# Performance work log

Hardware: AMD Instinct MI355X
Metric: run time of the kernel (lower is better)

Reference implementation:

```python
import jax, jax.numpy as jnp
import numpy as np
import math

EMB_ATOM = 256
PAIR_IN = 64
PAIR_OUT = 64
EMB_RBF = 16
N_ATOMS = 50000
N_EDGES = 1_600_000
KMAX = 32


def setup_inputs() -> dict:
    key = jax.random.key(0)
    ks = jax.random.split(key, 8)
    h = jax.random.normal(ks[0], (N_ATOMS, EMB_ATOM), dtype=jnp.float32)
    rad_basis = jax.random.normal(ks[1], (N_ATOMS, EMB_RBF, KMAX), dtype=jnp.float32)
    edge_index = jax.random.randint(ks[2], (2, N_EDGES), 0, N_ATOMS, dtype=jnp.int64)
    target_neighbor_idx = jax.random.randint(ks[3], (N_EDGES,), 0, KMAX, dtype=jnp.int64)
    # Learned parameters (Dense layers are bias-free); stored as [in, out].
    W_down = jax.random.normal(ks[4], (EMB_ATOM, PAIR_IN), dtype=jnp.float32) / math.sqrt(EMB_ATOM)
    W_bilinear = jax.random.normal(ks[5], (EMB_RBF * PAIR_IN, PAIR_OUT), dtype=jnp.float32) / math.sqrt(EMB_RBF * PAIR_IN)
    W_up = jax.random.normal(ks[6], (PAIR_OUT, EMB_ATOM), dtype=jnp.float32) / math.sqrt(PAIR_OUT)
    scale = jnp.ones((), dtype=jnp.float32)  # ScaleFactor learned scalar
    return {"h": h, "rad_basis": rad_basis, "edge_index": edge_index,
            "target_neighbor_idx": target_neighbor_idx, "W_down": W_down,
            "W_bilinear": W_bilinear, "W_up": W_up, "scale": scale}


def reference(h, rad_basis, edge_index, target_neighbor_idx, W_down, W_bilinear, W_up, scale):
    num_atoms = h.shape[0]
    kmax = rad_basis.shape[-1]
    pair_in = W_down.shape[-1]
    # down_projection (Dense, silu activation, no bias)
    x_b = jax.nn.silu(h @ W_down)                              # [N, pair_in]
    x_ba = x_b[edge_index[0]]                                  # [E, pair_in] gather by source atom
    # scatter edge features into padded per-atom neighbor buffer
    x2 = jnp.zeros((num_atoms, kmax, pair_in), dtype=x_ba.dtype)
    x2 = x2.at[edge_index[1], target_neighbor_idx].set(x_ba)   # [N, Kmax, pair_in]
    # rbf-weighted neighbor aggregation: batched matmul
    x_ba2 = jnp.einsum('nrk,nkd->nrd', rad_basis, x2)          # [N, rbf, pair_in]
    h_out = x_ba2.reshape(num_atoms, -1) @ W_bilinear          # bilinear Dense, no activation
    h_out = h_out * scale                                      # ScaleFactor
    return jax.nn.silu(h_out @ W_up)                           # up_projection
```

## Files before the change

kernel.cpp:

```cpp
#include <hip/hip_runtime.h>

typedef __attribute__((ext_vector_type(8))) short short8;
typedef __attribute__((ext_vector_type(4))) float floatx4;
typedef unsigned short u16;
typedef unsigned int u32;
typedef unsigned long long u64;

#define KMAXN 32

__device__ __forceinline__ u16 f2b(float f) {
    unsigned u = __builtin_bit_cast(unsigned, f);
    u += 0x7FFFu + ((u >> 16) & 1u);
    return (u16)(u >> 16);
}
__device__ __forceinline__ float silu_f(float x) {
    return x / (1.f + __expf(-x));
}

__global__ __launch_bounds__(256) void k_init(const float* __restrict__ Wd,
                                              const float* __restrict__ Wb,
                                              const float* __restrict__ Wu,
                                              u16* __restrict__ WdT,
                                              u16* __restrict__ WbT2,
                                              u16* __restrict__ WuT,
                                              u64* __restrict__ win64,
                                              int nslots) {
    long idx = (long)blockIdx.x * 256 + threadIdx.x;
    if (idx < 16384) {
        WdT[idx] = f2b(Wd[(idx & 255) * 64 + (idx >> 8)]);
    } else if (idx < 81920) {
        int i = (int)idx - 16384;
        int n = i >> 10, s = i & 1023;
        int d = s >> 4, rbf = s & 15;
        WbT2[i] = f2b(Wb[(rbf * 64 + d) * 64 + n]);
    } else if (idx < 98304) {
        int i = (int)idx - 81920;
        WuT[i] = f2b(Wu[(i & 63) * 256 + (i >> 6)]);
    } else {
        long z = idx - 98304;
        if (z < nslots / 2) {
            uint4 zero = {0, 0, 0, 0};
            reinterpret_cast<uint4*>(win64)[z] = zero;
        }
    }
}

__global__ __launch_bounds__(256) void k_prep(const float* __restrict__ h,
                                              const u16*   __restrict__ WdT,
                                              u16*         __restrict__ xb,
                                              const int*   __restrict__ esrc,
                                              const int*   __restrict__ edst,
                                              const int*   __restrict__ tni,
                                              u64*         __restrict__ win64,
                                              int E, int DOWN) {
    const int tid = threadIdx.x;
    if ((int)blockIdx.x >= DOWN) {
        int e = (blockIdx.x - DOWN) * 256 + tid;
        if (e < E) {
            u64 v = ((u64)(unsigned)(e + 1) << 32) | (u32)esrc[e];
            atomicMax(&win64[(long)edst[e] * KMAXN + tni[e]], v);
        }
        return;
    }
    const int wave = tid >> 6;
    const int lane = tid & 63;
    const int m = lane & 15;
    const int q = lane >> 4;
    const long atom0 = (long)blockIdx.x * 16;

    const float* arow = h + (atom0 + m) * 256 + q * 8;
    const u16* brow = WdT + (wave * 16 + m) * 256 + q * 8;
    floatx4 acc = {0.f, 0.f, 0.f, 0.f};
#pragma unroll
    for (int kk = 0; kk < 8; ++kk) {
        float4 f0 = *reinterpret_cast<const float4*>(arow + kk * 32);
        float4 f1 = *reinterpret_cast<const float4*>(arow + kk * 32 + 4);
        short8 a;
        a[0] = (short)f2b(f0.x); a[1] = (short)f2b(f0.y);
        a[2] = (short)f2b(f0.z); a[3] = (short)f2b(f0.w);
        a[4] = (short)f2b(f1.x); a[5] = (short)f2b(f1.y);
        a[6] = (short)f2b(f1.z); a[7] = (short)f2b(f1.w);
        short8 b = *reinterpret_cast<const short8*>(brow + kk * 32);
        acc = __builtin_amdgcn_mfma_f32_16x16x32_bf16(a, b, acc, 0, 0, 0);
    }
#pragma unroll
    for (int r = 0; r < 4; ++r) {
        xb[(atom0 + q * 4 + r) * 64 + wave * 16 + m] = f2b(silu_f(acc[r]));
    }
}

#define T_STRIDE 1032
#define X2_PAD   68

__global__ __launch_bounds__(256) void k_fused(
        const float* __restrict__ rad,
        const u16*   __restrict__ xb,
        const u64*   __restrict__ win64,
        const u16*   __restrict__ WbT2,
        const u16*   __restrict__ WuT,
        const float* __restrict__ scale_p,
        float* __restrict__ out) {
    __shared__ alignas(16) u16 t2[16][T_STRIDE];
    __shared__ alignas(16) u16 c2_lds[16][72];
    __shared__ alignas(16) u16 x2s[4][KMAXN][X2_PAD];

    const int tid  = threadIdx.x;
    const int wave = tid >> 6;
    const int lane = tid & 63;
    const int m = lane & 15;
    const int q = lane >> 4;
    const long atom0 = (long)blockIdx.x * 16;
    const long nbase = atom0 + wave * 4;

    const int slot = lane >> 1;
    const int half = lane & 1;

    int src[4];
#pragma unroll
    for (int a = 0; a < 4; ++a) {
        u64 w = win64[(nbase + a) * KMAXN + slot];
        src[a] = w ? (int)(u32)w : -1;
    }

    short8 ra[4];
#pragma unroll
    for (int a = 0; a < 4; ++a) {
        const float* rrow = rad + (nbase + a) * 512 + m * 32 + q * 8;
        float4 r0 = *reinterpret_cast<const float4*>(rrow);
        float4 r1 = *reinterpret_cast<const float4*>(rrow + 4);
        ra[a][0] = (short)f2b(r0.x); ra[a][1] = (short)f2b(r0.y);
        ra[a][2] = (short)f2b(r0.z); ra[a][3] = (short)f2b(r0.w);
        ra[a][4] = (short)f2b(r1.x); ra[a][5] = (short)f2b(r1.y);
        ra[a][6] = (short)f2b(r1.z); ra[a][7] = (short)f2b(r1.w);
    }

    uint4 g[4][4];
#pragma unroll
    for (int a = 0; a < 4; ++a) {
        if (src[a] >= 0) {
            const uint4* p = reinterpret_cast<const uint4*>(xb + (long)src[a] * 64 + half * 32);
            g[a][0] = p[0]; g[a][1] = p[1]; g[a][2] = p[2]; g[a][3] = p[3];
        } else {
            uint4 z = {0, 0, 0, 0};
            g[a][0] = z; g[a][1] = z; g[a][2] = z; g[a][3] = z;
        }
    }

#pragma unroll
    for (int a = 0; a < 4; ++a) {
        u64* d = reinterpret_cast<u64*>(&x2s[wave][slot][half * 32]);
        const u64* s = reinterpret_cast<const u64*>(&g[a][0]);
#pragma unroll
        for (int i = 0; i < 8; ++i) d[i] = s[i];
        asm volatile("s_waitcnt lgkmcnt(0)" ::: "memory");

#pragma unroll
        for (int c = 0; c < 4; ++c) {
            short8 bx;
#pragma unroll
            for (int j = 0; j < 8; ++j) {
                bx[j] = (short)x2s[wave][q * 8 + j][c * 16 + m];
            }
            floatx4 tz = {0.f, 0.f, 0.f, 0.f};
            tz = __builtin_amdgcn_mfma_f32_16x16x32_bf16(ra[a], bx, tz, 0, 0, 0);
            u32 lo = (u32)f2b(tz[0]) | ((u32)f2b(tz[1]) << 16);
            u32 hi = (u32)f2b(tz[2]) | ((u32)f2b(tz[3]) << 16);
            u64 val = (u64)lo | ((u64)hi << 32);
            *reinterpret_cast<u64*>(&t2[wave * 4 + a][(c * 16 + m) * 16 + q * 4]) = val;
        }
        asm volatile("" ::: "memory");
    }
    __syncthreads();

    floatx4 c2 = {0.f, 0.f, 0.f, 0.f};
    const u16* wbrow = WbT2 + (wave * 16 + m) * 1024 + q * 8;
#pragma unroll 4
    for (int kk = 0; kk < 32; ++kk) {
        short8 af = *reinterpret_cast<const short8*>(&t2[m][kk * 32 + q * 8]);
        short8 bf = *reinterpret_cast<const short8*>(wbrow + kk * 32);
        c2 = __builtin_amdgcn_mfma_f32_16x16x32_bf16(af, bf, c2, 0, 0, 0);
    }
    {
        float sc = scale_p[0];
#pragma unroll
        for (int r = 0; r < 4; ++r) {
            c2_lds[q * 4 + r][wave * 16 + m] = f2b(c2[r] * sc);
        }
    }
    __syncthreads();

#pragma unroll
    for (int tt = 0; tt < 4; ++tt) {
        floatx4 acc = {0.f, 0.f, 0.f, 0.f};
        const u16* wurow = WuT + (wave * 64 + tt * 16 + m) * 64 + q * 8;
#pragma unroll
        for (int ks = 0; ks < 2; ++ks) {
            short8 af = *reinterpret_cast<const short8*>(&c2_lds[m][ks * 32 + q * 8]);
            short8 bf = *reinterpret_cast<const short8*>(wurow + ks * 32);
            acc = __builtin_amdgcn_mfma_f32_16x16x32_bf16(af, bf, acc, 0, 0, 0);
        }
#pragma unroll
        for (int r = 0; r < 4; ++r) {
            out[(atom0 + q * 4 + r) * 256 + wave * 64 + tt * 16 + m] = silu_f(acc[r]);
        }
    }
}

extern "C" void kernel_launch(void* const* d_in, const int* in_sizes, int n_in,
                              void* d_out, int out_size, void* d_ws, size_t ws_size,
                              hipStream_t stream) {
    const float* h     = (const float*)d_in[0];
    const float* rad   = (const float*)d_in[1];
    const int*   eidx  = (const int*)d_in[2];
    const int*   tni   = (const int*)d_in[3];
    const float* Wd    = (const float*)d_in[4];
    const float* Wb    = (const float*)d_in[5];
    const float* Wu    = (const float*)d_in[6];
    const float* scale = (const float*)d_in[7];
    float* out         = (float*)d_out;

    const int E = in_sizes[3];
    const int N = in_sizes[0] / 256;
    const int nslots = N * KMAXN;

    u16* xb = (u16*)d_ws;
    size_t off = (size_t)N * 64 * sizeof(u16);
    u64* win64 = (u64*)((char*)d_ws + off);
    off += (size_t)nslots * sizeof(u64);
    u16* WdT  = (u16*)((char*)d_ws + off);  off += 16384 * 2;
    u16* WbT2 = (u16*)((char*)d_ws + off);  off += 65536 * 2;
    u16* WuT  = (u16*)((char*)d_ws + off);

    const int DOWN = N / 16;
    const int WIN  = (E + 255) / 256;
    const int INIT = 384 + (nslots / 2 + 255) / 256;

    k_init<<<INIT, 256, 0, stream>>>(Wd, Wb, Wu, WdT, WbT2, WuT, win64, nslots);
    k_prep<<<DOWN + WIN, 256, 0, stream>>>(h, WdT, xb, eidx, eidx + E, tni, win64, E, DOWN);
    k_fused<<<DOWN, 256, 0, stream>>>(rad, xb, win64, WbT2, WuT, scale, out);
}
```

Baseline: 350.8 us.

## Split fused kernel into two passes to halve LDS staging and raise occupancy

The neighbor-aggregation and bilinear stages now run in two passes over halves of the pair-feature columns. Each pass stages only half of the intermediate t2 tile in shared memory, and the gather registers are no longer kept for all four atoms at once. Launch bounds request four blocks per CU so more waves can hide gather latency. In exchange, each source row is gathered twice (the second time likely from cache), and an extra block barrier is added per pass.

```diff
diff --git a/kernel.cpp b/kernel.cpp
--- a/kernel.cpp
+++ b/kernel.cpp
@@ -89,10 +89,9 @@
     }
 }
 
-#define T_STRIDE 1032
 #define X2_PAD   68
 
-__global__ __launch_bounds__(256) void k_fused(
+__global__ __launch_bounds__(256, 4) void k_fused(
         const float* __restrict__ rad,
         const u16*   __restrict__ xb,
         const u64*   __restrict__ win64,
@@ -100,7 +99,7 @@
         const u16*   __restrict__ WuT,
         const float* __restrict__ scale_p,
         float* __restrict__ out) {
-    __shared__ alignas(16) u16 t2[16][T_STRIDE];
+    __shared__ alignas(16) u16 t2[16][520];
     __shared__ alignas(16) u16 c2_lds[16][72];
     __shared__ alignas(16) u16 x2s[4][KMAXN][X2_PAD];
 
@@ -111,7 +110,6 @@
     const int q = lane >> 4;
     const long atom0 = (long)blockIdx.x * 16;
     const long nbase = atom0 + wave * 4;
-
     const int slot = lane >> 1;
     const int half = lane & 1;
 
@@ -134,52 +132,59 @@
         ra[a][6] = (short)f2b(r1.z); ra[a][7] = (short)f2b(r1.w);
     }
 
-    uint4 g[4][4];
-#pragma unroll
-    for (int a = 0; a < 4; ++a) {
-        if (src[a] >= 0) {
-            const uint4* p = reinterpret_cast<const uint4*>(xb + (long)src[a] * 64 + half * 32);
-            g[a][0] = p[0]; g[a][1] = p[1]; g[a][2] = p[2]; g[a][3] = p[3];
-        } else {
-            uint4 z = {0, 0, 0, 0};
-            g[a][0] = z; g[a][1] = z; g[a][2] = z; g[a][3] = z;
-        }
-    }
-
-#pragma unroll
-    for (int a = 0; a < 4; ++a) {
-        u64* d = reinterpret_cast<u64*>(&x2s[wave][slot][half * 32]);
-        const u64* s = reinterpret_cast<const u64*>(&g[a][0]);
-#pragma unroll
-        for (int i = 0; i < 8; ++i) d[i] = s[i];
-        asm volatile("s_waitcnt lgkmcnt(0)" ::: "memory");
-
-#pragma unroll
-        for (int c = 0; c < 4; ++c) {
-            short8 bx;
-#pragma unroll
-            for (int j = 0; j < 8; ++j) {
-                bx[j] = (short)x2s[wave][q * 8 + j][c * 16 + m];
+    floatx4 c2 = {0.f, 0.f, 0.f, 0.f};
+
+    for (int pass = 0; pass < 2; ++pass) {
+        if (pass) __syncthreads();
+#pragma unroll
+        for (int a = 0; a < 4; ++a) {
+            uint4 g0, g1, g2, g3;
+            if (src[a] >= 0) {
+                const uint4* p = reinterpret_cast<const uint4*>(xb + (long)src[a] * 64 + half * 32);
+                g0 = p[0]; g1 = p[1]; g2 = p[2]; g3 = p[3];
+            } else {
+                uint4 z = {0, 0, 0, 0};
+                g0 = z; g1 = z; g2 = z; g3 = z;
             }
-            floatx4 tz = {0.f, 0.f, 0.f, 0.f};
-            tz = __builtin_amdgcn_mfma_f32_16x16x32_bf16(ra[a], bx, tz, 0, 0, 0);
-            u32 lo = (u32)f2b(tz[0]) | ((u32)f2b(tz[1]) << 16);
-            u32 hi = (u32)f2b(tz[2]) | ((u32)f2b(tz[3]) << 16);
-            u64 val = (u64)lo | ((u64)hi << 32);
-            *reinterpret_cast<u64*>(&t2[wave * 4 + a][(c * 16 + m) * 16 + q * 4]) = val;
-        }
-        asm volatile("" ::: "memory");
-    }
-    __syncthreads();
-
-    floatx4 c2 = {0.f, 0.f, 0.f, 0.f};
-    const u16* wbrow = WbT2 + (wave * 16 + m) * 1024 + q * 8;
+            {
+                u64* d = reinterpret_cast<u64*>(&x2s[wave][slot][half * 32]);
+                const u64* s = reinterpret_cast<const u64*>(&g0);
+                *reinterpret_cast<uint4*>(&x2s[wave][slot][half * 32])      = g0;
+                *reinterpret_cast<uint4*>(&x2s[wave][slot][half * 32 + 8])  = g1;
+                *reinterpret_cast<uint4*>(&x2s[wave][slot][half * 32 + 16]) = g2;
+                *reinterpret_cast<uint4*>(&x2s[wave][slot][half * 32 + 24]) = g3;
+                (void)d; (void)s;
+            }
+            asm volatile("s_waitcnt lgkmcnt(0)" ::: "memory");
+
+#pragma unroll
+            for (int cc = 0; cc < 2; ++cc) {
+                const int c = pass * 2 + cc;
+                short8 bx;
+#pragma unroll
+                for (int j = 0; j < 8; ++j) {
+                    bx[j] = (short)x2s[wave][q * 8 + j][c * 16 + m];
+                }
+                floatx4 tz = {0.f, 0.f, 0.f, 0.f};
+                tz = __builtin_amdgcn_mfma_f32_16x16x32_bf16(ra[a], bx, tz, 0, 0, 0);
+                u32 lo = (u32)f2b(tz[0]) | ((u32)f2b(tz[1]) << 16);
+                u32 hi = (u32)f2b(tz[2]) | ((u32)f2b(tz[3]) << 16);
+                u64 val = (u64)lo | ((u64)hi << 32);
+                *reinterpret_cast<u64*>(&t2[wave * 4 + a][(cc * 16 + m) * 16 + q * 4]) = val;
+            }
+            asm volatile("" ::: "memory");
+        }
+        __syncthreads();
+
+        const u16* wbrow = WbT2 + (wave * 16 + m) * 1024 + pass * 512 + q * 8;
 #pragma unroll 4
-    for (int kk = 0; kk < 32; ++kk) {
-        short8 af = *reinterpret_cast<const short8*>(&t2[m][kk * 32 + q * 8]);
-        short8 bf = *reinterpret_cast<const short8*>(wbrow + kk * 32);
-        c2 = __builtin_amdgcn_mfma_f32_16x16x32_bf16(af, bf, c2, 0, 0, 0);
-    }
+        for (int kk = 0; kk < 16; ++kk) {
+            short8 af = *reinterpret_cast<const short8*>(&t2[m][kk * 32 + q * 8]);
+            short8 bf = *reinterpret_cast<const short8*>(wbrow + kk * 32);
+            c2 = __builtin_amdgcn_mfma_f32_16x16x32_bf16(af, bf, c2, 0, 0, 0);
+        }
+    }
+
     {
         float sc = scale_p[0];
 #pragma unroll
```

New measurement: 360.7 us. +2.8%, slower.

## Gather neighbor features directly into MFMA operands, dropping LDS staging

Applied to the files above, without the earlier changes.

Removes the per-wave LDS staging buffer for gathered neighbor rows. Each lane now reads its 8 neighbor slot indices with vector loads and fetches single bf16 elements from global xb straight into the MFMA B operand. Empty slots point at a zeroed sentinel row appended after xb, which removes the branch. Launch bounds now request 4 blocks per CU. The cost is many scattered 2-byte global loads in place of coalesced 16-byte loads, traded for less LDS traffic, fewer waits and higher occupancy.

```diff
diff --git a/kernel.cpp b/kernel.cpp
--- a/kernel.cpp
+++ b/kernel.cpp
@@ -24,6 +24,7 @@
                                               u16* __restrict__ WbT2,
                                               u16* __restrict__ WuT,
                                               u64* __restrict__ win64,
+                                              u16* __restrict__ xb,
                                               int nslots) {
     long idx = (long)blockIdx.x * 256 + threadIdx.x;
     if (idx < 16384) {
@@ -38,9 +39,13 @@
         WuT[i] = f2b(Wu[(i & 63) * 256 + (i >> 6)]);
     } else {
         long z = idx - 98304;
+        uint4 zero = {0, 0, 0, 0};
         if (z < nslots / 2) {
-            uint4 zero = {0, 0, 0, 0};
             reinterpret_cast<uint4*>(win64)[z] = zero;
+            if (z < 8) {
+                long N = nslots / KMAXN;
+                reinterpret_cast<uint4*>(xb + N * 64)[z] = zero;
+            }
         }
     }
 }
@@ -90,19 +95,18 @@
 }
 
 #define T_STRIDE 1032
-#define X2_PAD   68
-
-__global__ __launch_bounds__(256) void k_fused(
+
+__global__ __launch_bounds__(256, 4) void k_fused(
         const float* __restrict__ rad,
         const u16*   __restrict__ xb,
         const u64*   __restrict__ win64,
         const u16*   __restrict__ WbT2,
         const u16*   __restrict__ WuT,
         const float* __restrict__ scale_p,
-        float* __restrict__ out) {
+        float* __restrict__ out,
+        int N) {
     __shared__ alignas(16) u16 t2[16][T_STRIDE];
     __shared__ alignas(16) u16 c2_lds[16][72];
-    __shared__ alignas(16) u16 x2s[4][KMAXN][X2_PAD];
 
     const int tid  = threadIdx.x;
     const int wave = tid >> 6;
@@ -111,16 +115,6 @@
     const int q = lane >> 4;
     const long atom0 = (long)blockIdx.x * 16;
     const long nbase = atom0 + wave * 4;
-
-    const int slot = lane >> 1;
-    const int half = lane & 1;
-
-    int src[4];
-#pragma unroll
-    for (int a = 0; a < 4; ++a) {
-        u64 w = win64[(nbase + a) * KMAXN + slot];
-        src[a] = w ? (int)(u32)w : -1;
-    }
 
     short8 ra[4];
 #pragma unroll
@@ -134,33 +128,40 @@
         ra[a][6] = (short)f2b(r1.z); ra[a][7] = (short)f2b(r1.w);
     }
 
-    uint4 g[4][4];
 #pragma unroll
     for (int a = 0; a < 4; ++a) {
-        if (src[a] >= 0) {
-            const uint4* p = reinterpret_cast<const uint4*>(xb + (long)src[a] * 64 + half * 32);
-            g[a][0] = p[0]; g[a][1] = p[1]; g[a][2] = p[2]; g[a][3] = p[3];
-        } else {
-            uint4 z = {0, 0, 0, 0};
-            g[a][0] = z; g[a][1] = z; g[a][2] = z; g[a][3] = z;
-        }
-    }
-
-#pragma unroll
-    for (int a = 0; a < 4; ++a) {
-        u64* d = reinterpret_cast<u64*>(&x2s[wave][slot][half * 32]);
-        const u64* s = reinterpret_cast<const u64*>(&g[a][0]);
-#pragma unroll
-        for (int i = 0; i < 8; ++i) d[i] = s[i];
-        asm volatile("s_waitcnt lgkmcnt(0)" ::: "memory");
-
+        const u64* wp = win64 + (nbase + a) * KMAXN + q * 8;
+        uint4 w0 = *reinterpret_cast<const uint4*>(wp);
+        uint4 w1 = *reinterpret_cast<const uint4*>(wp + 2);
+        uint4 w2 = *reinterpret_cast<const uint4*>(wp + 4);
+        uint4 w3 = *reinterpret_cast<const uint4*>(wp + 6);
+        int s0 = w0.y ? (int)w0.x : N;
+        int s1 = w0.w ? (int)w0.z : N;
+        int s2 = w1.y ? (int)w1.x : N;
+        int s3 = w1.w ? (int)w1.z : N;
+        int s4 = w2.y ? (int)w2.x : N;
+        int s5 = w2.w ? (int)w2.z : N;
+        int s6 = w3.y ? (int)w3.x : N;
+        int s7 = w3.w ? (int)w3.z : N;
+        const u16* rp0 = xb + (long)s0 * 64 + m;
+        const u16* rp1 = xb + (long)s1 * 64 + m;
+        const u16* rp2 = xb + (long)s2 * 64 + m;
+        const u16* rp3 = xb + (long)s3 * 64 + m;
+        const u16* rp4 = xb + (long)s4 * 64 + m;
+        const u16* rp5 = xb + (long)s5 * 64 + m;
+        const u16* rp6 = xb + (long)s6 * 64 + m;
+        const u16* rp7 = xb + (long)s7 * 64 + m;
 #pragma unroll
         for (int c = 0; c < 4; ++c) {
             short8 bx;
-#pragma unroll
-            for (int j = 0; j < 8; ++j) {
-                bx[j] = (short)x2s[wave][q * 8 + j][c * 16 + m];
-            }
+            bx[0] = (short)rp0[c * 16];
+            bx[1] = (short)rp1[c * 16];
+            bx[2] = (short)rp2[c * 16];
+            bx[3] = (short)rp3[c * 16];
+            bx[4] = (short)rp4[c * 16];
+            bx[5] = (short)rp5[c * 16];
+            bx[6] = (short)rp6[c * 16];
+            bx[7] = (short)rp7[c * 16];
             floatx4 tz = {0.f, 0.f, 0.f, 0.f};
             tz = __builtin_amdgcn_mfma_f32_16x16x32_bf16(ra[a], bx, tz, 0, 0, 0);
             u32 lo = (u32)f2b(tz[0]) | ((u32)f2b(tz[1]) << 16);
@@ -168,7 +169,6 @@
             u64 val = (u64)lo | ((u64)hi << 32);
             *reinterpret_cast<u64*>(&t2[wave * 4 + a][(c * 16 + m) * 16 + q * 4]) = val;
         }
-        asm volatile("" ::: "memory");
     }
     __syncthreads();
 
@@ -224,7 +224,7 @@
     const int nslots = N * KMAXN;
 
     u16* xb = (u16*)d_ws;
-    size_t off = (size_t)N * 64 * sizeof(u16);
+    size_t off = (size_t)(N + 1) * 64 * sizeof(u16);
     u64* win64 = (u64*)((char*)d_ws + off);
     off += (size_t)nslots * sizeof(u64);
     u16* WdT  = (u16*)((char*)d_ws + off);  off += 16384 * 2;
@@ -235,7 +235,7 @@
     const int WIN  = (E + 255) / 256;
     const int INIT = 384 + (nslots / 2 + 255) / 256;
 
-    k_init<<<INIT, 256, 0, stream>>>(Wd, Wb, Wu, WdT, WbT2, WuT, win64, nslots);
+    k_init<<<INIT, 256, 0, stream>>>(Wd, Wb, Wu, WdT, WbT2, WuT, win64, xb, nslots);
     k_prep<<<DOWN + WIN, 256, 0, stream>>>(h, WdT, xb, eidx, eidx + E, tni, win64, E, DOWN);
-    k_fused<<<DOWN, 256, 0, stream>>>(rad, xb, win64, WbT2, WuT, scale, out);
-}
+    k_fused<<<DOWN, 256, 0, stream>>>(rad, xb, win64, WbT2, WuT, scale, out, N);
+}
```

Measured after the change: 360.5 us. +2.8%, slower.

## Gather neighbor features directly into MFMA operand registers, dropping LDS staging

Applied to the files above, without the earlier changes.

The fused kernel now loads each atom's 32 neighbor-winner slots as vectors, maps empty slots to a zero row appended after xb (zeroed in k_init), and gathers individual bf16 elements from global memory straight into MFMA B-operand layout. This removes the per-wave LDS staging buffer, its transpose reads and the lgkmcnt waits, and it sets launch bounds to two blocks per CU. The cost is many more small 2-byte scattered global loads per lane instead of 16-byte vector loads, plus higher register pressure from holding all gathered values.

```diff
diff --git a/kernel.cpp b/kernel.cpp
--- a/kernel.cpp
+++ b/kernel.cpp
@@ -24,6 +24,7 @@
                                               u16* __restrict__ WbT2,
                                               u16* __restrict__ WuT,
                                               u64* __restrict__ win64,
+                                              u16* __restrict__ xb,
                                               int nslots) {
     long idx = (long)blockIdx.x * 256 + threadIdx.x;
     if (idx < 16384) {
@@ -38,9 +39,13 @@
         WuT[i] = f2b(Wu[(i & 63) * 256 + (i >> 6)]);
     } else {
         long z = idx - 98304;
+        uint4 zero = {0, 0, 0, 0};
         if (z < nslots / 2) {
-            uint4 zero = {0, 0, 0, 0};
             reinterpret_cast<uint4*>(win64)[z] = zero;
+            if (z < 8) {
+                long N = nslots / KMAXN;
+                reinterpret_cast<uint4*>(xb + N * 64)[z] = zero;
+            }
         }
     }
 }
@@ -90,19 +95,18 @@
 }
 
 #define T_STRIDE 1032
-#define X2_PAD   68
-
-__global__ __launch_bounds__(256) void k_fused(
+
+__global__ __launch_bounds__(256, 2) void k_fused(
         const float* __restrict__ rad,
         const u16*   __restrict__ xb,
         const u64*   __restrict__ win64,
         const u16*   __restrict__ WbT2,
         const u16*   __restrict__ WuT,
         const float* __restrict__ scale_p,
-        float* __restrict__ out) {
+        float* __restrict__ out,
+        int N) {
     __shared__ alignas(16) u16 t2[16][T_STRIDE];
     __shared__ alignas(16) u16 c2_lds[16][72];
-    __shared__ alignas(16) u16 x2s[4][KMAXN][X2_PAD];
 
     const int tid  = threadIdx.x;
     const int wave = tid >> 6;
@@ -112,63 +116,69 @@
     const long atom0 = (long)blockIdx.x * 16;
     const long nbase = atom0 + wave * 4;
 
-    const int slot = lane >> 1;
-    const int half = lane & 1;
-
-    int src[4];
-#pragma unroll
-    for (int a = 0; a < 4; ++a) {
-        u64 w = win64[(nbase + a) * KMAXN + slot];
-        src[a] = w ? (int)(u32)w : -1;
-    }
-
+    uint4 w[4][4];
+#pragma unroll
+    for (int a = 0; a < 4; ++a) {
+        const uint4* wp = reinterpret_cast<const uint4*>(win64 + (nbase + a) * KMAXN + q * 8);
+#pragma unroll
+        for (int i = 0; i < 4; ++i) w[a][i] = wp[i];
+    }
+    float4 rf[4][2];
+#pragma unroll
+    for (int a = 0; a < 4; ++a) {
+        const float* rrow = rad + (nbase + a) * 512 + m * 32 + q * 8;
+        rf[a][0] = *reinterpret_cast<const float4*>(rrow);
+        rf[a][1] = *reinterpret_cast<const float4*>(rrow + 4);
+    }
+    u32 off[4][8];
+#pragma unroll
+    for (int a = 0; a < 4; ++a) {
+        off[a][0] = (w[a][0].y ? w[a][0].x : (u32)N) * 64u + (u32)m;
+        off[a][1] = (w[a][0].w ? w[a][0].z : (u32)N) * 64u + (u32)m;
+        off[a][2] = (w[a][1].y ? w[a][1].x : (u32)N) * 64u + (u32)m;
+        off[a][3] = (w[a][1].w ? w[a][1].z : (u32)N) * 64u + (u32)m;
+        off[a][4] = (w[a][2].y ? w[a][2].x : (u32)N) * 64u + (u32)m;
+        off[a][5] = (w[a][2].w ? w[a][2].z : (u32)N) * 64u + (u32)m;
+        off[a][6] = (w[a][3].y ? w[a][3].x : (u32)N) * 64u + (u32)m;
+        off[a][7] = (w[a][3].w ? w[a][3].z : (u32)N) * 64u + (u32)m;
+    }
+    u32 gv[4][8][4];
+#pragma unroll
+    for (int a = 0; a < 4; ++a) {
+#pragma unroll
+        for (int j = 0; j < 8; ++j) {
+            const u16* p = xb + off[a][j];
+#pragma unroll
+            for (int c = 0; c < 4; ++c) {
+                gv[a][j][c] = (u32)p[c * 16];
+            }
+        }
+    }
     short8 ra[4];
 #pragma unroll
     for (int a = 0; a < 4; ++a) {
-        const float* rrow = rad + (nbase + a) * 512 + m * 32 + q * 8;
-        float4 r0 = *reinterpret_cast<const float4*>(rrow);
-        float4 r1 = *reinterpret_cast<const float4*>(rrow + 4);
-        ra[a][0] = (short)f2b(r0.x); ra[a][1] = (short)f2b(r0.y);
-        ra[a][2] = (short)f2b(r0.z); ra[a][3] = (short)f2b(r0.w);
-        ra[a][4] = (short)f2b(r1.x); ra[a][5] = (short)f2b(r1.y);
-        ra[a][6] = (short)f2b(r1.z); ra[a][7] = (short)f2b(r1.w);
-    }
-
-    uint4 g[4][4];
-#pragma unroll
-    for (int a = 0; a < 4; ++a) {
-        if (src[a] >= 0) {
-            const uint4* p = reinterpret_cast<const uint4*>(xb + (long)src[a] * 64 + half * 32);
-            g[a][0] = p[0]; g[a][1] = p[1]; g[a][2] = p[2]; g[a][3] = p[3];
-        } else {
-            uint4 z = {0, 0, 0, 0};
-            g[a][0] = z; g[a][1] = z; g[a][2] = z; g[a][3] = z;
-        }
-    }
-
-#pragma unroll
-    for (int a = 0; a < 4; ++a) {
-        u64* d = reinterpret_cast<u64*>(&x2s[wave][slot][half * 32]);
-        const u64* s = reinterpret_cast<const u64*>(&g[a][0]);
-#pragma unroll
-        for (int i = 0; i < 8; ++i) d[i] = s[i];
-        asm volatile("s_waitcnt lgkmcnt(0)" ::: "memory");
-
+        ra[a][0] = (short)f2b(rf[a][0].x); ra[a][1] = (short)f2b(rf[a][0].y);
+        ra[a][2] = (short)f2b(rf[a][0].z); ra[a][3] = (short)f2b(rf[a][0].w);
+        ra[a][4] = (short)f2b(rf[a][1].x); ra[a][5] = (short)f2b(rf[a][1].y);
+        ra[a][6] = (short)f2b(rf[a][1].z); ra[a][7] = (short)f2b(rf[a][1].w);
+    }
+
+#pragma unroll
+    for (int a = 0; a < 4; ++a) {
 #pragma unroll
         for (int c = 0; c < 4; ++c) {
-            short8 bx;
-#pragma unroll
-            for (int j = 0; j < 8; ++j) {
-                bx[j] = (short)x2s[wave][q * 8 + j][c * 16 + m];
-            }
+            union { u32 u[4]; short8 s; } bx;
+            bx.u[0] = (gv[a][0][c] & 0xffffu) | (gv[a][1][c] << 16);
+            bx.u[1] = (gv[a][2][c] & 0xffffu) | (gv[a][3][c] << 16);
+            bx.u[2] = (gv[a][4][c] & 0xffffu) | (gv[a][5][c] << 16);
+            bx.u[3] = (gv[a][6][c] & 0xffffu) | (gv[a][7][c] << 16);
             floatx4 tz = {0.f, 0.f, 0.f, 0.f};
-            tz = __builtin_amdgcn_mfma_f32_16x16x32_bf16(ra[a], bx, tz, 0, 0, 0);
+            tz = __builtin_amdgcn_mfma_f32_16x16x32_bf16(ra[a], bx.s, tz, 0, 0, 0);
             u32 lo = (u32)f2b(tz[0]) | ((u32)f2b(tz[1]) << 16);
             u32 hi = (u32)f2b(tz[2]) | ((u32)f2b(tz[3]) << 16);
             u64 val = (u64)lo | ((u64)hi << 32);
             *reinterpret_cast<u64*>(&t2[wave * 4 + a][(c * 16 + m) * 16 + q * 4]) = val;
         }
-        asm volatile("" ::: "memory");
     }
     __syncthreads();
 
@@ -224,7 +234,7 @@
     const int nslots = N * KMAXN;
 
     u16* xb = (u16*)d_ws;
-    size_t off = (size_t)N * 64 * sizeof(u16);
+    size_t off = (size_t)(N + 1) * 64 * sizeof(u16);
     u64* win64 = (u64*)((char*)d_ws + off);
     off += (size_t)nslots * sizeof(u64);
     u16* WdT  = (u16*)((char*)d_ws + off);  off += 16384 * 2;
@@ -235,7 +245,7 @@
     const int WIN  = (E + 255) / 256;
     const int INIT = 384 + (nslots / 2 + 255) / 256;
 
-    k_init<<<INIT, 256, 0, stream>>>(Wd, Wb, Wu, WdT, WbT2, WuT, win64, nslots);
+    k_init<<<INIT, 256, 0, stream>>>(Wd, Wb, Wu, WdT, WbT2, WuT, win64, xb, nslots);
     k_prep<<<DOWN + WIN, 256, 0, stream>>>(h, WdT, xb, eidx, eidx + E, tni, win64, E, DOWN);
-    k_fused<<<DOWN, 256, 0, stream>>>(rad, xb, win64, WbT2, WuT, scale, out);
-}
+    k_fused<<<DOWN, 256, 0, stream>>>(rad, xb, win64, WbT2, WuT, scale, out, N);
+}
```

Result: no change. 356.0 us (+1.5%).
